# Kernel optimization log

Hardware: AMD Instinct MI355X
Metric: run time of the kernel (lower is better)

Reference implementation:

```python
import jax, jax.numpy as jnp
import numpy as np

N_HEADS = 6
N_POINTS = 4
EPS = 1e-6


def layer_norm(x, g, b):
    m = jnp.mean(x, axis=-1, keepdims=True)
    v = jnp.var(x, axis=-1, keepdims=True)
    return (x - m) * jax.lax.rsqrt(v + EPS) * g + b


def bilinear_sample(value_l, h, w, loc):
    """value_l: (B, h*w, H, Dh); loc: (B, Lq, H, P, 2) normalized to [0,1].
    grid_sample semantics: align_corners=False, padding_mode='zeros'.
    Returns (B, H, Lq, P, Dh)."""
    B, HW, Hh, Dh = value_l.shape
    Lq, P = loc.shape[1], loc.shape[3]
    v = jnp.transpose(value_l, (0, 2, 1, 3))  # (B,H,HW,Dh)
    x = loc[..., 0] * w - 0.5
    y = loc[..., 1] * h - 0.5
    x0 = jnp.floor(x)
    y0 = jnp.floor(y)
    wx = x - x0
    wy = y - y0

    def gather(xi, yi):
        valid = (xi >= 0) & (xi < w) & (yi >= 0) & (yi < h)
        xc = jnp.clip(xi, 0, w - 1).astype(jnp.int32)
        yc = jnp.clip(yi, 0, h - 1).astype(jnp.int32)
        idx = yc * w + xc  # (B,Lq,H,P)
        idx_t = jnp.transpose(idx, (0, 2, 1, 3)).reshape(B, Hh, Lq * P)
        g = jnp.take_along_axis(v, idx_t[..., None], axis=2)  # (B,H,Lq*P,Dh)
        g = g.reshape(B, Hh, Lq, P, Dh)
        m = jnp.transpose(valid, (0, 2, 1, 3))[..., None].astype(g.dtype)
        return g * m

    g00 = gather(x0, y0)
    g01 = gather(x0 + 1, y0)
    g10 = gather(x0, y0 + 1)
    g11 = gather(x0 + 1, y0 + 1)
    wx_t = jnp.transpose(wx, (0, 2, 1, 3))[..., None]
    wy_t = jnp.transpose(wy, (0, 2, 1, 3))[..., None]
    top = g00 * (1 - wx_t) + g01 * wx_t
    bot = g10 * (1 - wx_t) + g11 * wx_t
    return top * (1 - wy_t) + bot * wy_t


def ms_deform_attn(qn, ref, feat_n, Wv, bv, Woff, boff, Waw, baw, Wout, bout, shapes, starts):
    B, Lq, C = qn.shape
    Hh, P, Lv = N_HEADS, N_POINTS, len(shapes)
    Dh = C // Hh
    value = (feat_n @ Wv + bv).reshape(B, -1, Hh, Dh)
    off = (qn @ Woff + boff).reshape(B, Lq, Hh, Lv, P, 2)
    aw = (qn @ Waw + baw).reshape(B, Lq, Hh, Lv * P)
    aw = jax.nn.softmax(aw, axis=-1).reshape(B, Lq, Hh, Lv, P)
    # offset normalizer is [W, H] per level
    normalizer = jnp.asarray([[w_, h_] for (h_, w_) in shapes], dtype=qn.dtype)
    loc = ref[:, :, None, :, None, :] + off / normalizer[None, None, None, :, None, :]
    out = 0.0
    for l, (h_, w_) in enumerate(shapes):
        value_l = jax.lax.dynamic_slice_in_dim(value, starts[l], h_ * w_, axis=1)
        sampled = bilinear_sample(value_l, h_, w_, loc[:, :, :, l])  # (B,H,Lq,P,Dh)
        out = out + jnp.einsum('bhqpd,bqhp->bqhd', sampled, aw[:, :, :, l])
    out = out.reshape(B, Lq, C)
    return out @ Wout + bout


def setup_inputs() -> dict:
    key = jax.random.key(0)
    ks = jax.random.split(key, 12)
    B, Lq, C, M = 2, 4096, 384, 4
    H, P, Lv = N_HEADS, N_POINTS, 1
    s = 0.02
    inp = {}
    inp['query'] = jax.random.normal(ks[0], (B, Lq, C), jnp.float32)
    inp['reference_points'] = jax.random.uniform(ks[1], (B, Lq, Lv, 2), jnp.float32)
    inp['feat'] = jax.random.normal(ks[2], (B, Lq, C), jnp.float32)
    inp['feat_other'] = jax.random.normal(ks[3], (M - 1, B, Lq, C), jnp.float32)
    inp['qn_g'] = jnp.ones((C,), jnp.float32)
    inp['qn_b'] = jnp.zeros((C,), jnp.float32)
    inp['fn_g'] = jnp.ones((M, C), jnp.float32)
    inp['fn_b'] = jnp.zeros((M, C), jnp.float32)
    inp['Wv'] = jax.random.normal(ks[4], (M, C, C), jnp.float32) * s
    inp['bv'] = jnp.zeros((M, C), jnp.float32)
    inp['Woff'] = jax.random.normal(ks[5], (M, C, H * Lv * P * 2), jnp.float32) * s
    inp['boff'] = jax.random.normal(ks[6], (M, H * Lv * P * 2), jnp.float32) * 0.5
    inp['Waw'] = jax.random.normal(ks[7], (M, C, H * Lv * P), jnp.float32) * s
    inp['baw'] = jnp.zeros((M, H * Lv * P), jnp.float32)
    inp['Wout'] = jax.random.normal(ks[8], (M, C, C), jnp.float32) * s
    inp['bout'] = jnp.zeros((M, C), jnp.float32)
    inp['gamma'] = jax.random.normal(ks[9], (M, C), jnp.float32) * 0.1
    inp['spatial_shapes'] = np.array([[64, 64]], dtype=np.int64)
    inp['level_start_index'] = np.array([0], dtype=np.int64)
    return inp


def reference(query, reference_points, feat, feat_other, qn_g, qn_b, fn_g, fn_b,
              Wv, bv, Woff, boff, Waw, baw, Wout, bout, gamma,
              spatial_shapes, level_start_index):
    shapes = [(int(h), int(w)) for h, w in np.asarray(spatial_shapes)]
    starts = [int(v) for v in np.asarray(level_start_index)]
    qn = layer_norm(query, qn_g, qn_b)
    feats = [feat] + [feat_other[i] for i in range(feat_other.shape[0])]
    out = query
    for m in range(len(feats)):
        fn = layer_norm(feats[m], fn_g[m], fn_b[m])
        attn = ms_deform_attn(qn, reference_points, fn,
                              Wv[m], bv[m], Woff[m], boff[m],
                              Waw[m], baw[m], Wout[m], bout[m], shapes, starts)
        out = out + gamma[m] * attn
    return out
```

## Files before the change

kernel.cpp:

```cpp
#include <hip/hip_runtime.h>
#include <hip/hip_bf16.h>

#define RTOT 8192
#define C_   384
#define M_   4
#define H_   6
#define P_   4
#define KOUT 1536

typedef __bf16 bf16;
typedef bf16  bf16x8 __attribute__((ext_vector_type(8)));
typedef float f32x4  __attribute__((ext_vector_type(4)));

#define GLOAD_LDS16(g, l) __builtin_amdgcn_global_load_lds( \
    (const __attribute__((address_space(1))) unsigned int*)(g), \
    (__attribute__((address_space(3))) unsigned int*)(l), 16, 0, 0)

#define S0 589824
#define S1 786432
#define S2 1376256
#define S3 1376768
#define S4 1377152

__global__ __launch_bounds__(256) void cvt_kernel(
    const float* __restrict__ Wv, const float* __restrict__ Woff,
    const float* __restrict__ Waw, const float* __restrict__ Wout,
    const float* __restrict__ gamma, const float* __restrict__ boff,
    const float* __restrict__ baw, const float* __restrict__ bout,
    bf16* __restrict__ WvT, bf16* __restrict__ WoffawT, bf16* __restrict__ WoutT,
    float* __restrict__ oabias, float* __restrict__ boutbig)
{
    for (int idx = blockIdx.x * 256 + threadIdx.x; idx < S4; idx += gridDim.x * 256) {
        if (idx < S0) {
            int t = idx; int m = t / (C_ * C_); int rr = t % (C_ * C_);
            int n = rr / C_, k = rr % C_;
            WvT[t] = (bf16)Wv[(size_t)m * C_ * C_ + (size_t)k * C_ + n];
        } else if (idx < S1) {
            int t = idx - S0; int m = t / (128 * C_); int rr = t % (128 * C_);
            int n = rr / C_, k = rr % C_;
            float v = 0.f;
            if (n < 48)      v = Woff[(size_t)m * C_ * 48 + (size_t)k * 48 + n];
            else if (n < 72) v = Waw[(size_t)m * C_ * 24 + (size_t)k * 24 + (n - 48)];
            WoffawT[t] = (bf16)v;
        } else if (idx < S2) {
            int t = idx - S1; int n = t / KOUT; int kk = t % KOUT;
            int m = kk / C_, k = kk % C_;
            WoutT[t] = (bf16)(Wout[(size_t)m * C_ * C_ + (size_t)k * C_ + n] * gamma[m * C_ + n]);
        } else if (idx < S3) {
            int t = idx - S2; int m = t / 128; int n = t % 128;
            float v = 0.f;
            if (n < 48)      v = boff[m * 48 + n];
            else if (n < 72) v = baw[m * 24 + (n - 48)];
            oabias[t] = v;
        } else {
            int c = idx - S3;
            float s = 0.f;
            for (int m = 0; m < M_; ++m) s += gamma[m * C_ + c] * bout[m * C_ + c];
            boutbig[c] = s;
        }
    }
}

__global__ __launch_bounds__(256) void ln_kernel(
    const float* __restrict__ query, const float* __restrict__ feat,
    const float* __restrict__ feat_other,
    const float* __restrict__ qn_g, const float* __restrict__ qn_b,
    const float* __restrict__ fn_g, const float* __restrict__ fn_b,
    bf16* __restrict__ qn, bf16* __restrict__ fn)
{
    const int r = blockIdx.x * 4 + (threadIdx.x >> 6);
    const int which = blockIdx.y;
    const int lane = threadIdx.x & 63;
    const float* src; const float* g; const float* bb; bf16* dst;
    if (which == 0) { src = query; g = qn_g; bb = qn_b; dst = qn; }
    else {
        int m = which - 1;
        src = (m == 0) ? feat : feat_other + (size_t)(m - 1) * RTOT * C_;
        g = fn_g + m * C_; bb = fn_b + m * C_; dst = fn + (size_t)m * RTOT * C_;
    }
    src += (size_t)r * C_; dst += (size_t)r * C_;
    float v[6]; float s = 0.f, sq = 0.f;
#pragma unroll
    for (int j = 0; j < 6; ++j) {
        v[j] = src[lane + j * 64];
        s += v[j]; sq += v[j] * v[j];
    }
#pragma unroll
    for (int o = 1; o < 64; o <<= 1) {
        s += __shfl_xor(s, o);
        sq += __shfl_xor(sq, o);
    }
    const float mean = s * (1.f / C_);
    const float var  = sq * (1.f / C_) - mean * mean;
    const float rs   = rsqrtf(var + 1e-6f);
#pragma unroll
    for (int j = 0; j < 6; ++j) {
        int c = lane + j * 64;
        dst[c] = (bf16)((v[j] - mean) * rs * g[c] + bb[c]);
    }
}

template <int MODE>
__global__ __launch_bounds__(256) void gemm_kernel(
    const bf16* __restrict__ A, long long aStride,
    const bf16* __restrict__ W, long long wStride,
    const float* __restrict__ bias, int biasStride,
    const float* __restrict__ extra,
    void* __restrict__ OutP, long long oStride,
    int K, int ldo)
{
    __shared__ __align__(16) bf16 As[2][64 * 32];
    __shared__ __align__(16) bf16 Bs[2][64 * 32];
    const int mb = blockIdx.z;
    A += (long long)mb * aStride;
    W += (long long)mb * wStride;
    bias += mb * biasStride;
    const int brow = blockIdx.x * 64;
    const int bcol = blockIdx.y * 64;
    const int tid = threadIdx.x;
    const int lane = tid & 63;
    const int wave = tid >> 6;
    const int wr = wave >> 1, wc = wave & 1;
    const int lr = lane & 15, lg = lane >> 4;

    const int r0 = tid >> 2, s0 = tid & 3;
    const long long aoff = (long long)(brow + r0) * K + (s0 ^ ((r0 >> 1) & 3)) * 8;
    const long long boff = (long long)(bcol + r0) * K + (s0 ^ ((r0 >> 1) & 3)) * 8;

    int aRd[2], bRd[2];
#pragma unroll
    for (int i = 0; i < 2; ++i) {
        const int ra = wr * 32 + i * 16 + lr;
        const int rb = wc * 32 + i * 16 + lr;
        aRd[i] = ra * 32 + (lg ^ ((ra >> 1) & 3)) * 8;
        bRd[i] = rb * 32 + (lg ^ ((rb >> 1) & 3)) * 8;
    }

    f32x4 acc[2][2] = {};

    GLOAD_LDS16(A + aoff, (char*)&As[0][0] + tid * 16);
    GLOAD_LDS16(W + boff, (char*)&Bs[0][0] + tid * 16);
    __syncthreads();

    int cur = 0;
    for (int k0 = 0; k0 < K; k0 += 32) {
        if (k0 + 32 < K) {
            const int nb = cur ^ 1;
            GLOAD_LDS16(A + aoff + k0 + 32, (char*)&As[nb][0] + tid * 16);
            GLOAD_LDS16(W + boff + k0 + 32, (char*)&Bs[nb][0] + tid * 16);
        }
        bf16x8 af[2], bfr[2];
#pragma unroll
        for (int mi = 0; mi < 2; ++mi)
            af[mi] = *reinterpret_cast<const bf16x8*>(&As[cur][aRd[mi]]);
#pragma unroll
        for (int ni = 0; ni < 2; ++ni)
            bfr[ni] = *reinterpret_cast<const bf16x8*>(&Bs[cur][bRd[ni]]);
#pragma unroll
        for (int mi = 0; mi < 2; ++mi)
#pragma unroll
            for (int ni = 0; ni < 2; ++ni)
                acc[mi][ni] = __builtin_amdgcn_mfma_f32_16x16x32_bf16(
                    af[mi], bfr[ni], acc[mi][ni], 0, 0, 0);
        __syncthreads();
        cur ^= 1;
    }

#pragma unroll
    for (int mi = 0; mi < 2; ++mi) {
#pragma unroll
        for (int ni = 0; ni < 2; ++ni) {
#pragma unroll
            for (int rr = 0; rr < 4; ++rr) {
                int row = brow + wr * 32 + mi * 16 + lg * 4 + rr;
                int col = bcol + wc * 32 + ni * 16 + lr;
                float v = acc[mi][ni][rr] + bias[col];
                long long o = (long long)mb * oStride + (long long)row * ldo + col;
                if (MODE == 0)      ((bf16*)OutP)[o] = (bf16)v;
                else if (MODE == 1) ((float*)OutP)[o] = v;
                else                ((float*)OutP)[o] = v + extra[(long long)row * ldo + col];
            }
        }
    }
}

struct WP { float w; int off; };

__global__ __launch_bounds__(384) void sample_kernel(
    const float* __restrict__ offaw, const float* __restrict__ ref,
    const bf16* __restrict__ value, bf16* __restrict__ attn)
{
    const int bid   = blockIdx.x;
    const int combo = bid & 7;
    const int pair  = bid >> 3;
    const int m = combo >> 1, b = combo & 1;
    const int r0 = b * 4096 + pair * 2;

    __shared__ WP wp_s[2][24][4];

    const int t = threadIdx.x;
    if (t < 48) {
        const int row = t / 24;
        const int i   = t % 24;
        const int h = i >> 2, p = i & 3;
        const int r = r0 + row;
        const float* oa = offaw + ((long long)m * RTOT + r) * 128;
        float e = oa[48 + h * 4 + p];
        float mx = fmaxf(e, __shfl_xor(e, 1));
        mx = fmaxf(mx, __shfl_xor(mx, 2));
        float ex = expf(e - mx);
        float s = ex;
        s += __shfl_xor(s, 1);
        s += __shfl_xor(s, 2);
        const float aw = ex / s;
        const float x = ref[r * 2 + 0] * 64.f - 0.5f + oa[h * 8 + p * 2 + 0];
        const float y = ref[r * 2 + 1] * 64.f - 0.5f + oa[h * 8 + p * 2 + 1];
        const float xf = floorf(x), yf = floorf(y);
        const float wx = x - xf, wy = y - yf;
        const int x0 = (int)xf, y0 = (int)yf;
        const bool xok0 = (x0 >= 0) && (x0 < 64);
        const bool xok1 = (x0 >= -1) && (x0 < 63);
        const bool yok0 = (y0 >= 0) && (y0 < 64);
        const bool yok1 = (y0 >= -1) && (y0 < 63);
        const int xc0 = min(max(x0, 0), 63),     xc1 = min(max(x0 + 1, 0), 63);
        const int yc0 = min(max(y0, 0), 63),     yc1 = min(max(y0 + 1, 0), 63);
        WP w0 = { aw * (1.f - wx) * (1.f - wy) * (float)(xok0 && yok0), (yc0 * 64 + xc0) * (C_ * 2) };
        WP w1 = { aw * wx         * (1.f - wy) * (float)(xok1 && yok0), (yc0 * 64 + xc1) * (C_ * 2) };
        WP w2 = { aw * (1.f - wx) * wy         * (float)(xok0 && yok1), (yc1 * 64 + xc0) * (C_ * 2) };
        WP w3 = { aw * wx         * wy         * (float)(xok1 && yok1), (yc1 * 64 + xc1) * (C_ * 2) };
        wp_s[row][i][0] = w0;  wp_s[row][i][1] = w1;
        wp_s[row][i][2] = w2;  wp_s[row][i][3] = w3;
    }
    __syncthreads();

    const int row = t / 192;
    const int tl  = t % 192;
    const int h   = tl >> 5;
    const int l32 = tl & 31;
    const int r   = r0 + row;
    const char* vb = (const char*)(value
        + ((long long)m * RTOT + (long long)b * 4096) * C_ + h * 64 + l32 * 2);

    float wreg[16]; int oreg[16]; unsigned int vreg[16];
#pragma unroll
    for (int i = 0; i < 16; ++i) {
        WP wp = wp_s[row][h * 4 + (i >> 2)][i & 3];
        wreg[i] = wp.w; oreg[i] = wp.off;
    }
#pragma unroll
    for (int i = 0; i < 16; ++i)
        vreg[i] = *reinterpret_cast<const unsigned int*>(vb + oreg[i]);
    float acc0 = 0.f, acc1 = 0.f;
#pragma unroll
    for (int i = 0; i < 16; ++i) {
        unsigned int u = vreg[i];
        float lo = __builtin_bit_cast(float, u << 16);
        float hi = __builtin_bit_cast(float, u & 0xffff0000u);
        acc0 += wreg[i] * lo;
        acc1 += wreg[i] * hi;
    }
    union { bf16 h2[2]; unsigned int u; } o;
    o.h2[0] = (bf16)acc0; o.h2[1] = (bf16)acc1;
    *reinterpret_cast<unsigned int*>(attn + (long long)r * KOUT + m * C_ + h * 64 + l32 * 2) = o.u;
}

extern "C" void kernel_launch(void* const* d_in, const int* in_sizes, int n_in,
                              void* d_out, int out_size, void* d_ws, size_t ws_size,
                              hipStream_t stream)
{
    const float* query      = (const float*)d_in[0];
    const float* ref        = (const float*)d_in[1];
    const float* feat       = (const float*)d_in[2];
    const float* feat_other = (const float*)d_in[3];
    const float* qn_g = (const float*)d_in[4];
    const float* qn_b = (const float*)d_in[5];
    const float* fn_g = (const float*)d_in[6];
    const float* fn_b = (const float*)d_in[7];
    const float* Wv   = (const float*)d_in[8];
    const float* bv   = (const float*)d_in[9];
    const float* Woff = (const float*)d_in[10];
    const float* boff = (const float*)d_in[11];
    const float* Waw  = (const float*)d_in[12];
    const float* baw  = (const float*)d_in[13];
    const float* Wout = (const float*)d_in[14];
    const float* bout = (const float*)d_in[15];
    const float* gamma = (const float*)d_in[16];
    float* out = (float*)d_out;

    char* ws = (char*)d_ws;
    size_t off = 0;
    auto carve = [&](size_t bytes) { char* p = ws + off; off += (bytes + 255) & ~(size_t)255; return p; };
    bf16*  qn      = (bf16*)carve((size_t)RTOT * C_ * 2);
    bf16*  fn      = (bf16*)carve((size_t)M_ * RTOT * C_ * 2);
    bf16*  value   = (bf16*)carve((size_t)M_ * RTOT * C_ * 2);
    bf16*  attn    = (bf16*)carve((size_t)RTOT * KOUT * 2);
    float* offaw   = (float*)carve((size_t)M_ * RTOT * 128 * 4);
    bf16*  WvT     = (bf16*)carve((size_t)M_ * C_ * C_ * 2);
    bf16*  WoffawT = (bf16*)carve((size_t)M_ * 128 * C_ * 2);
    bf16*  WoutT   = (bf16*)carve((size_t)C_ * KOUT * 2);
    float* oabias  = (float*)carve((size_t)M_ * 128 * 4);
    float* boutbig = (float*)carve((size_t)C_ * 4);

    cvt_kernel<<<512, 256, 0, stream>>>(Wv, Woff, Waw, Wout, gamma, boff, baw, bout,
                                        WvT, WoffawT, WoutT, oabias, boutbig);
    ln_kernel<<<dim3(RTOT / 4, 5), 256, 0, stream>>>(query, feat, feat_other,
                                                     qn_g, qn_b, fn_g, fn_b, qn, fn);
    gemm_kernel<0><<<dim3(RTOT / 64, C_ / 64, M_), 256, 0, stream>>>(
        fn, (long long)RTOT * C_, WvT, (long long)C_ * C_, bv, C_, nullptr,
        value, (long long)RTOT * C_, C_, C_);
    gemm_kernel<1><<<dim3(RTOT / 64, 2, M_), 256, 0, stream>>>(
        qn, 0LL, WoffawT, (long long)128 * C_, oabias, 128, nullptr,
        offaw, (long long)RTOT * 128, C_, 128);
    sample_kernel<<<dim3(RTOT * M_ / 2), 384, 0, stream>>>(offaw, ref, value, attn);
    gemm_kernel<2><<<dim3(RTOT / 64, C_ / 64, 1), 256, 0, stream>>>(
        attn, 0LL, WoutT, 0LL, boutbig, 0, query,
        out, 0LL, KOUT, C_);
}
```

Measured before the change: 120.1 us.

## Deepen GEMM LDS pipeline to five stages with explicit vmcnt waits

Replaces the double-buffered LDS staging in the MFMA GEMM with a five-buffer ring that keeps four k-tiles of global-to-LDS loads in flight. Each iteration uses a combined s_waitcnt vmcnt plus s_barrier that waits only on the oldest outstanding tile, instead of a full __syncthreads after every tile. The goal is to hide global memory latency behind the MFMA work. The cost is more LDS per block (20 KB versus 8 KB), which may lower occupancy, and the correctness now depends on hand-counted vmcnt values.

```diff
diff --git a/kernel.cpp b/kernel.cpp
--- a/kernel.cpp
+++ b/kernel.cpp
@@ -15,6 +15,10 @@
 #define GLOAD_LDS16(g, l) __builtin_amdgcn_global_load_lds( \
     (const __attribute__((address_space(1))) unsigned int*)(g), \
     (__attribute__((address_space(3))) unsigned int*)(l), 16, 0, 0)
+
+#define WAITB(N) do { \
+    asm volatile("s_waitcnt vmcnt(" #N ")\n\ts_barrier" ::: "memory"); \
+    __builtin_amdgcn_sched_barrier(0); } while (0)
 
 #define S0 589824
 #define S1 786432
@@ -109,8 +113,8 @@
     void* __restrict__ OutP, long long oStride,
     int K, int ldo)
 {
-    __shared__ __align__(16) bf16 As[2][64 * 32];
-    __shared__ __align__(16) bf16 Bs[2][64 * 32];
+    __shared__ __align__(16) bf16 As[5][64 * 32];
+    __shared__ __align__(16) bf16 Bs[5][64 * 32];
     const int mb = blockIdx.z;
     A += (long long)mb * aStride;
     W += (long long)mb * wStride;
@@ -136,34 +140,43 @@
         bRd[i] = rb * 32 + (lg ^ ((rb >> 1) & 3)) * 8;
     }
 
+    const int nk = K >> 5;
     f32x4 acc[2][2] = {};
 
-    GLOAD_LDS16(A + aoff, (char*)&As[0][0] + tid * 16);
-    GLOAD_LDS16(W + boff, (char*)&Bs[0][0] + tid * 16);
-    __syncthreads();
-
-    int cur = 0;
-    for (int k0 = 0; k0 < K; k0 += 32) {
-        if (k0 + 32 < K) {
-            const int nb = cur ^ 1;
-            GLOAD_LDS16(A + aoff + k0 + 32, (char*)&As[nb][0] + tid * 16);
-            GLOAD_LDS16(W + boff + k0 + 32, (char*)&Bs[nb][0] + tid * 16);
-        }
+#pragma unroll
+    for (int t = 0; t < 4; ++t) {
+        GLOAD_LDS16(A + aoff + t * 32, (char*)&As[t][0] + tid * 16);
+        GLOAD_LDS16(W + boff + t * 32, (char*)&Bs[t][0] + tid * 16);
+    }
+
+    int cb = 0;
+    int ib = 4;
+    for (int kt = 0; kt < nk; ++kt) {
+        if (kt + 4 < nk) {
+            WAITB(6);
+            GLOAD_LDS16(A + aoff + (kt + 4) * 32, (char*)&As[ib][0] + tid * 16);
+            GLOAD_LDS16(W + boff + (kt + 4) * 32, (char*)&Bs[ib][0] + tid * 16);
+        } else if (kt + 4 == nk) { WAITB(6); }
+        else if (kt + 3 == nk)   { WAITB(4); }
+        else if (kt + 2 == nk)   { WAITB(2); }
+        else                     { WAITB(0); }
+
         bf16x8 af[2], bfr[2];
 #pragma unroll
         for (int mi = 0; mi < 2; ++mi)
-            af[mi] = *reinterpret_cast<const bf16x8*>(&As[cur][aRd[mi]]);
+            af[mi] = *reinterpret_cast<const bf16x8*>(&As[cb][aRd[mi]]);
 #pragma unroll
         for (int ni = 0; ni < 2; ++ni)
-            bfr[ni] = *reinterpret_cast<const bf16x8*>(&Bs[cur][bRd[ni]]);
+            bfr[ni] = *reinterpret_cast<const bf16x8*>(&Bs[cb][bRd[ni]]);
 #pragma unroll
         for (int mi = 0; mi < 2; ++mi)
 #pragma unroll
             for (int ni = 0; ni < 2; ++ni)
                 acc[mi][ni] = __builtin_amdgcn_mfma_f32_16x16x32_bf16(
                     af[mi], bfr[ni], acc[mi][ni], 0, 0, 0);
-        __syncthreads();
-        cur ^= 1;
+
+        cb = (cb == 4) ? 0 : cb + 1;
+        ib = (ib == 4) ? 0 : ib + 1;
     }
 
 #pragma unroll
```

Result: no change. 121.7 us (+1.3%).
